# Optimization experiments

Hardware: AMD Instinct MI355X
Metric: run time of the kernel (lower is better)

## Reference

```python
import jax, jax.numpy as jnp
import numpy as np
import math

B, N, D, H, K, W = 2, 2048, 512, 8, 64, 5
HD = D // H      # head_dim = 64
QC = HD // 4     # per-head quaternion component = 16
QI = D // 4      # full-model quaternion component = 128


def _qlinear(x, r, i, j, k, b):
    # Hamilton-product weight matrix, as built in QLinear.forward
    Wm = jnp.concatenate([
        jnp.concatenate([r, -i, -j, -k], 1),
        jnp.concatenate([i,  r, -k,  j], 1),
        jnp.concatenate([j,  k,  r, -i], 1),
        jnp.concatenate([k, -j,  i,  r], 1)], 0)
    return x @ Wm.T + b


def _layernorm(x, g, b, eps=1e-5):
    m = x.mean(-1, keepdims=True)
    v = ((x - m) ** 2).mean(-1, keepdims=True)
    return (x - m) / jnp.sqrt(v + eps) * g + b


def _forward(query, key, value, cross_context, density_feat, mask, time_idx,
             q_r, q_i, q_j, q_k, q_b, k_r, k_i, k_j, k_k, k_b,
             v_w, v_b, o_w, o_b, thr, dm1_w, dm1_b, dm2_w, dm2_b,
             ef, ec, ev_w, ev_b, ln_g, ln_b):
    spike_slope = 5.0
    # ---- QuaternionSpikeAttention (cross_ctx=True, dropout inactive in eval) ----
    q = _qlinear(query, q_r, q_i, q_j, q_k, q_b)
    k = _qlinear(key, k_r, k_i, k_j, k_k, k_b) + _qlinear(cross_context, k_r, k_i, k_j, k_k, k_b)
    v = jnp.concatenate([value, cross_context], -1) @ v_w.T + v_b
    qh = q.reshape(B, N, H, HD)
    kh = k.reshape(B, N, H, HD)
    vh = v.reshape(B, N, H, HD)
    # sum of the 4 quaternion-component dot products == full dot over head_dim
    scores = jnp.einsum('bmhd,bnhd->bhmn', qh, kh) / math.sqrt(QC)
    scores = jnp.clip(scores, -6.0, 6.0)
    base_thr = jax.nn.softplus(thr)
    hdm = jax.nn.gelu(density_feat @ dm1_w.T + dm1_b, approximate=False)
    d_shift = (hdm @ dm2_w.T + dm2_b)[..., 0]                # [B, N]
    threshold = base_thr + d_shift[:, None, None, :] * 0.1   # varies over key index
    gate = jax.nn.sigmoid(spike_slope * (scores - threshold))
    mod = scores * (1.0 + 2.0 * gate)
    m2 = mask[:, None, :, None] * mask[:, None, None, :]     # [B,1,M,N] outer mask
    mod = jnp.where(m2 == 0, -10000.0, mod)
    wts = jax.nn.softmax(jnp.clip(mod, -30.0, 30.0), axis=-1)
    attn = jnp.einsum('bhmn,bnhd->bmhd', wts, vh).reshape(B, N, D)
    attn = attn @ o_w.T + o_b
    # ---- TemporalEventConvolution ----
    order = jnp.argsort(time_idx, axis=1)
    qs = jnp.take_along_axis(query, order[..., None], axis=1)
    ms = jnp.take_along_axis(mask, order, axis=1)
    half = W // 2
    qp = jnp.pad(qs, ((0, 0), (half, half), (0, 0)))
    qwin = jnp.stack([qp[:, w:w + N] for w in range(W)], axis=2)  # [B,N,W,D]
    # quaternion-split filter matching collapses to a full dot over D
    act = jnp.einsum('bnwd,kwd->bnk', qwin, ef) / math.sqrt(QI)
    act = jnp.where(ms[..., None] == 0, -10000.0, act)
    act = jax.nn.softmax(act, axis=-1)
    ctx = act @ ec                                            # [B,N,D]
    ctx = _layernorm(ctx @ ev_w.T + ev_b, ln_g, ln_b) * ms[..., None]
    inv = jnp.argsort(order, axis=1)
    ctx = jnp.take_along_axis(ctx, inv[..., None], axis=1) * mask[..., None]
    return attn + ctx


def setup_inputs() -> dict:
    key0 = jax.random.key(0)
    ks = jax.random.split(key0, 24)
    lim = math.sqrt(6.0 / (QI + QI))
    def xav(k):
        return jax.random.uniform(k, (QI, QI), jnp.float32, -lim, lim)
    def lin(k, o, i):
        l = math.sqrt(1.0 / i)
        return jax.random.uniform(k, (o, i), jnp.float32, -l, l)
    return {
        'query': jax.random.normal(ks[0], (B, N, D), jnp.float32),
        'key': jax.random.normal(ks[1], (B, N, D), jnp.float32),
        'value': jax.random.normal(ks[2], (B, N, D), jnp.float32),
        'cross_context': jax.random.normal(ks[3], (B, N, D), jnp.float32),
        'density_feat': jax.random.normal(ks[4], (B, N, 3), jnp.float32),
        'mask': jnp.ones((B, N), jnp.float32),
        'time_idx': jax.random.randint(ks[5], (B, N), 0, 1000000),
        'q_r': xav(ks[6]), 'q_i': xav(ks[7]), 'q_j': xav(ks[8]), 'q_k': xav(ks[9]),
        'q_b': jnp.zeros((D,), jnp.float32),
        'k_r': xav(ks[10]), 'k_i': xav(ks[11]), 'k_j': xav(ks[12]), 'k_k': xav(ks[13]),
        'k_b': jnp.zeros((D,), jnp.float32),
        'v_w': lin(ks[14], D, 2 * D), 'v_b': jnp.zeros((D,), jnp.float32),
        'o_w': lin(ks[15], D, D), 'o_b': jnp.zeros((D,), jnp.float32),
        'thr': jnp.float32(-1.0),
        'dm1_w': lin(ks[16], 16, 3), 'dm1_b': jnp.zeros((16,), jnp.float32),
        'dm2_w': jnp.zeros((1, 16), jnp.float32), 'dm2_b': jnp.zeros((1,), jnp.float32),
        'ef': jax.random.normal(ks[17], (K, W, D), jnp.float32) * 0.02,
        'ec': jax.random.normal(ks[18], (K, D), jnp.float32) * 0.02,
        'ev_w': lin(ks[19], D, D), 'ev_b': jnp.zeros((D,), jnp.float32),
        'ln_g': jnp.ones((D,), jnp.float32), 'ln_b': jnp.zeros((D,), jnp.float32),
    }


def reference(query, key, value, cross_context, density_feat, mask, time_idx,
              q_r, q_i, q_j, q_k, q_b, k_r, k_i, k_j, k_k, k_b,
              v_w, v_b, o_w, o_b, thr, dm1_w, dm1_b, dm2_w, dm2_b,
              ef, ec, ev_w, ev_b, ln_g, ln_b):
    return _forward(query, key, value, cross_context, density_feat, mask, time_idx,
                    q_r, q_i, q_j, q_k, q_b, k_r, k_i, k_j, k_k, k_b,
                    v_w, v_b, o_w, o_b, thr, dm1_w, dm1_b, dm2_w, dm2_b,
                    ef, ec, ev_w, ev_b, ln_g, ln_b)
```

## Files before the change

### kernel.cpp

```cpp
#include <hip/hip_runtime.h>
#include <math.h>

#define BB 2
#define NN 2048
#define DDIM 512
#define HH 8
#define HDIM 64
#define BN 4096

#define WS_WMQ   0
#define WS_WMK   262144
#define WS_THRK  524288
#define WS_ORDER 528384
#define WS_DKW   532480
#define WS_W5    1843200
#define WS_Q     2105344
#define WS_K     4202496
#define WS_V     6299648
#define PLANE_US 2097152

typedef short bf16x8 __attribute__((ext_vector_type(8)));
typedef float f32x4  __attribute__((ext_vector_type(4)));

__device__ __forceinline__ float4 ld4(const float* p) { return *(const float4*)p; }

__device__ __forceinline__ float red16_sum(float v) {
  v += __shfl_xor(v, 1, 64);
  v += __shfl_xor(v, 2, 64);
  v += __shfl_xor(v, 4, 64);
  v += __shfl_xor(v, 8, 64);
  return v;
}

__device__ __forceinline__ unsigned short f2bu(float f) {
  unsigned u = __float_as_uint(f);
  unsigned r = 0x7FFFu + ((u >> 16) & 1u);
  return (unsigned short)((u + r) >> 16);
}
__device__ __forceinline__ float bu2f(unsigned short u) {
  return __uint_as_float(((unsigned)u) << 16);
}
__device__ __forceinline__ void split2(float x, unsigned short& hi, unsigned short& lo) {
  hi = f2bu(x);
  lo = f2bu(x - bu2f(hi));
}

__global__ __launch_bounds__(256) void build_wm_kernel(
    const float* __restrict__ qr, const float* __restrict__ qi,
    const float* __restrict__ qj, const float* __restrict__ qk,
    const float* __restrict__ kr, const float* __restrict__ ki,
    const float* __restrict__ kj, const float* __restrict__ kk,
    unsigned short* __restrict__ wmqH, unsigned short* __restrict__ wmqL,
    unsigned short* __restrict__ wmkH, unsigned short* __restrict__ wmkL)
{
  int idx = blockIdx.x * 256 + threadIdx.x;
  int sel = idx >> 18;
  int r   = idx & 262143;
  int p = r >> 9, q = r & 511;
  int pb = p >> 7, qb = q >> 7, pr = p & 127, qc = q & 127;
  const int   comp_t[4][4] = {{0,1,2,3},{1,0,3,2},{2,3,0,1},{3,2,1,0}};
  const float sign_t[4][4] = {{1.f,-1.f,-1.f,-1.f},{1.f,1.f,-1.f,1.f},
                              {1.f,1.f,1.f,-1.f},{1.f,-1.f,1.f,1.f}};
  const float* cq[4] = {qr,qi,qj,qk};
  const float* ck[4] = {kr,ki,kj,kk};
  int c = comp_t[pb][qb];
  float s = sign_t[pb][qb];
  const float* src = sel ? ck[c] : cq[c];
  float v = s * src[pr*128 + qc];
  unsigned short hi, lo;
  split2(v, hi, lo);
  if (sel) { wmkH[r] = hi; wmkL[r] = lo; }
  else     { wmqH[r] = hi; wmqL[r] = lo; }
}

__global__ __launch_bounds__(256) void presplit_kernel(
    const float* __restrict__ src, int n4,
    unsigned short* __restrict__ hp, unsigned short* __restrict__ lp)
{
  int i = blockIdx.x * 256 + threadIdx.x;
  if (i >= n4) return;
  float4 v = ((const float4*)src)[i];
  ushort4 h, l;
  split2(v.x, h.x, l.x);  split2(v.y, h.y, l.y);
  split2(v.z, h.z, l.z);  split2(v.w, h.w, l.w);
  ((ushort4*)hp)[i] = h;
  ((ushort4*)lp)[i] = l;
}

__global__ __launch_bounds__(256) void rank_kernel(const int* __restrict__ tidx,
                                                   int* __restrict__ order)
{
  __shared__ int ts[NN];
  int b = blockIdx.y;
  for (int i = threadIdx.x; i < NN; i += 256) ts[i] = tidx[b*NN + i];
  __syncthreads();
  int i = blockIdx.x * 256 + threadIdx.x;
  int ti = ts[i];
  int rank = 0;
  #pragma unroll 4
  for (int j = 0; j < NN; j++) {
    int tj = ts[j];
    rank += (tj < ti || (tj == ti && j < i)) ? 1 : 0;
  }
  order[b*NN + rank] = i;
}

__global__ __launch_bounds__(256) void thr_kernel(
    const float* __restrict__ df, const float* __restrict__ dm1w,
    const float* __restrict__ dm1b, const float* __restrict__ dm2w,
    const float* __restrict__ dm2b, const float* __restrict__ thrp,
    int dm1b_bstride, float* __restrict__ thrK)
{
  int i = blockIdx.x * 256 + threadIdx.x;
  if (i >= BN) return;
  int b = i >> 11;
  const float* bb = dm1b + b*dm1b_bstride;
  float x0 = df[i*3+0], x1 = df[i*3+1], x2 = df[i*3+2];
  float acc = dm2b[0];
  #pragma unroll
  for (int j = 0; j < 16; j++) {
    float h = dm1w[j*3+0]*x0 + dm1w[j*3+1]*x1 + dm1w[j*3+2]*x2 + bb[j];
    h = 0.5f * h * (1.f + erff(h * 0.70710678118654752f));
    acc += h * dm2w[j];
  }
  float tv = thrp[0];
  float base = fmaxf(tv, 0.f) + log1pf(expf(-fabsf(tv)));
  thrK[i] = base + 0.1f * acc;
}

#define GSTR 72
template<int MODE, int OUT, int AP, int BP>
__device__ __forceinline__ void mgemm_body(
    unsigned short* AHi, unsigned short* ALo,
    unsigned short* BHi, unsigned short* BLo,
    const float* __restrict__ A0, const float* __restrict__ A1,
    const unsigned short* __restrict__ APh, const unsigned short* __restrict__ APl,
    const float* __restrict__ W,
    const unsigned short* __restrict__ BPh, const unsigned short* __restrict__ BPl,
    const float* __restrict__ bias,
    float bias_scale, float scale, float* __restrict__ out,
    int Ka, int N, int ldout, int bx, int by)
{
  const int t = threadIdx.x;
  const int w = t >> 6, lane = t & 63;
  const int quad = lane >> 4, lm = lane & 15;
  const int m0 = bx * 64, n0 = by * 64;
  const int lrr = t >> 4, ld = (t & 15) * 4;

  f32x4 acc[4];
  #pragma unroll
  for (int s = 0; s < 4; s++) acc[s] = (f32x4){0.f,0.f,0.f,0.f};

  for (int k0 = 0; k0 < Ka; k0 += 64) {
    __syncthreads();
    if (AP) {
      #pragma unroll
      for (int i = 0; i < 2; i++) {
        int c = t*2 + i;
        int row = c >> 3, c8 = (c & 7) * 8;
        int off = (m0 + row)*Ka + k0 + c8;
        *(uint4*)&AHi[row*GSTR + c8] = *(const uint4*)&APh[off];
        *(uint4*)&ALo[row*GSTR + c8] = *(const uint4*)&APl[off];
      }
    } else {
      #pragma unroll
      for (int p = 0; p < 4; p++) {
        int row = lrr + p*16;
        float4 av;
        if (MODE == 0) {
          av = ld4(&A0[(size_t)(m0+row)*Ka + k0 + ld]);
        } else if (MODE == 1) {
          float4 x = ld4(&A0[(m0+row)*512 + k0 + ld]);
          float4 y = ld4(&A1[(m0+row)*512 + k0 + ld]);
          av = make_float4(x.x+y.x, x.y+y.y, x.z+y.z, x.w+y.w);
        } else {
          int kg = k0 + ld;
          av = (kg < 512) ? ld4(&A0[(m0+row)*512 + kg])
                          : ld4(&A1[(m0+row)*512 + kg - 512]);
        }
        ushort4 hi, lo;
        split2(av.x, hi.x, lo.x);  split2(av.y, hi.y, lo.y);
        split2(av.z, hi.z, lo.z);  split2(av.w, hi.w, lo.w);
        *(ushort4*)&AHi[row*GSTR + ld] = hi;
        *(ushort4*)&ALo[row*GSTR + ld] = lo;
      }
    }
    if (BP) {
      #pragma unroll
      for (int i = 0; i < 2; i++) {
        int c = t*2 + i;
        int row = c >> 3, c8 = (c & 7) * 8;
        int brow = n0 + row;  if (brow > N-1) brow = N-1;
        int off = brow*Ka + k0 + c8;
        *(uint4*)&BHi[row*GSTR + c8] = *(const uint4*)&BPh[off];
        *(uint4*)&BLo[row*GSTR + c8] = *(const uint4*)&BPl[off];
      }
    } else {
      #pragma unroll
      for (int p = 0; p < 4; p++) {
        int row = lrr + p*16;
        int brow = n0 + row;  if (brow > N-1) brow = N-1;
        float4 wv = ld4(&W[(size_t)brow*Ka + k0 + ld]);
        ushort4 hi, lo;
        split2(wv.x, hi.x, lo.x);  split2(wv.y, hi.y, lo.y);
        split2(wv.z, hi.z, lo.z);  split2(wv.w, hi.w, lo.w);
        *(ushort4*)&BHi[row*GSTR + ld] = hi;
        *(ushort4*)&BLo[row*GSTR + ld] = lo;
      }
    }
    __syncthreads();
    #pragma unroll
    for (int ks = 0; ks < 2; ks++) {
      int arow = (w*16 + lm)*GSTR + ks*32 + quad*8;
      bf16x8 ah = *(const bf16x8*)&AHi[arow];
      bf16x8 al = *(const bf16x8*)&ALo[arow];
      #pragma unroll
      for (int sub = 0; sub < 4; sub++) {
        int baddr = (sub*16 + lm)*GSTR + ks*32 + quad*8;
        bf16x8 bh = *(const bf16x8*)&BHi[baddr];
        bf16x8 bl = *(const bf16x8*)&BLo[baddr];
        acc[sub] = __builtin_amdgcn_mfma_f32_16x16x32_bf16(ah, bh, acc[sub], 0, 0, 0);
        acc[sub] = __builtin_amdgcn_mfma_f32_16x16x32_bf16(ah, bl, acc[sub], 0, 0, 0);
        acc[sub] = __builtin_amdgcn_mfma_f32_16x16x32_bf16(al, bh, acc[sub], 0, 0, 0);
      }
    }
  }
  #pragma unroll
  for (int sub = 0; sub < 4; sub++) {
    int col = n0 + sub*16 + lm;
    if (col >= N) continue;
    float bv = bias ? bias[col] * bias_scale : 0.f;
    if (OUT == 0) {
      #pragma unroll
      for (int r = 0; r < 4; r++) {
        int row = m0 + w*16 + quad*4 + r;
        out[(size_t)row*ldout + col] = acc[sub][r]*scale + bv;
      }
    } else if (OUT == 1) {
      unsigned short* hp = (unsigned short*)out;
      unsigned short* lp = hp + (size_t)4096*ldout;
      #pragma unroll
      for (int r = 0; r < 4; r++) {
        int row = m0 + w*16 + quad*4 + r;
        unsigned short hv, lv;
        split2(acc[sub][r]*scale + bv, hv, lv);
        hp[(size_t)row*ldout + col] = hv;
        lp[(size_t)row*ldout + col] = lv;
      }
    } else {
      unsigned short* hp = (unsigned short*)out;
      unsigned short* lp = hp + (size_t)PLANE_US;
      int hcol = col >> 6, d = col & 63;
      int row0 = m0 + w*16 + quad*4;
      int bb2 = row0 >> 11, n = row0 & 2047;
      unsigned short h0,h1,h2,h3,l0,l1,l2,l3;
      split2(acc[sub][0]*scale + bv, h0, l0);
      split2(acc[sub][1]*scale + bv, h1, l1);
      split2(acc[sub][2]*scale + bv, h2, l2);
      split2(acc[sub][3]*scale + bv, h3, l3);
      size_t vidx = (((size_t)bb2*8 + hcol)*64 + d)*2048 + n;
      *(ushort4*)&hp[vidx] = make_ushort4(h0,h1,h2,h3);
      *(ushort4*)&lp[vidx] = make_ushort4(l0,l1,l2,l3);
    }
  }
}

template<int MODE, int OUT, int AP, int BP>
__global__ __launch_bounds__(256) void mgemm_kernel(
    const float* __restrict__ A0, const float* __restrict__ A1,
    const unsigned short* __restrict__ APh, const unsigned short* __restrict__ APl,
    const float* __restrict__ W,
    const unsigned short* __restrict__ BPh, const unsigned short* __restrict__ BPl,
    const float* __restrict__ bias,
    float bias_scale, float scale, float* __restrict__ out,
    int Ka, int N, int ldout)
{
  __shared__ __align__(16) unsigned short AHi[64*GSTR], ALo[64*GSTR];
  __shared__ __align__(16) unsigned short BHi[64*GSTR], BLo[64*GSTR];
  mgemm_body<MODE,OUT,AP,BP>(AHi, ALo, BHi, BLo, A0, A1, APh, APl, W, BPh, BPl,
                             bias, bias_scale, scale, out, Ka, N, ldout,
                             blockIdx.x, blockIdx.y);
}

__global__ __launch_bounds__(256) void qkv_kernel(
    const unsigned short* __restrict__ qryH, const unsigned short* __restrict__ qryL,
    const unsigned short* __restrict__ wmqH, const unsigned short* __restrict__ wmqL,
    const float* __restrict__ q_b, float* __restrict__ Qb,
    const float* __restrict__ key_, const float* __restrict__ cross,
    const unsigned short* __restrict__ wmkH, const unsigned short* __restrict__ wmkL,
    const float* __restrict__ k_b, float* __restrict__ Kb,
    const float* __restrict__ value,
    const unsigned short* __restrict__ vwH, const unsigned short* __restrict__ vwL,
    const float* __restrict__ v_b, float* __restrict__ Vb)
{
  __shared__ __align__(16) unsigned short AHi[64*GSTR], ALo[64*GSTR];
  __shared__ __align__(16) unsigned short BHi[64*GSTR], BLo[64*GSTR];
  int by = blockIdx.y;
  if (by < 8) {
    mgemm_body<0,1,1,1>(AHi, ALo, BHi, BLo, nullptr, nullptr, qryH, qryL,
                        nullptr, wmqH, wmqL, q_b, 1.f, 1.f, Qb, 512, 512, 512,
                        blockIdx.x, by);
  } else if (by < 16) {
    mgemm_body<1,1,0,1>(AHi, ALo, BHi, BLo, key_, cross, nullptr, nullptr,
                        nullptr, wmkH, wmkL, k_b, 2.f, 1.f, Kb, 512, 512, 512,
                        blockIdx.x, by - 8);
  } else {
    mgemm_body<2,2,0,1>(AHi, ALo, BHi, BLo, value, cross, nullptr, nullptr,
                        nullptr, vwH, vwL, v_b, 1.f, 1.f, Vb, 1024, 512, 512,
                        blockIdx.x, by - 16);
  }
}

__global__ __launch_bounds__(256) void t1a_kernel(const float* __restrict__ dkw,
    const int* __restrict__ order, int K, int W, float* __restrict__ w5raw)
{
  int idx = blockIdx.x * 256 + threadIdx.x;
  if (idx >= BN*K) return;
  int k  = idx % K;
  int bn = idx / K;
  int b = bn >> 11, r = bn & 2047;
  const int* ob = order + b*NN;
  int KW = K*W, half = W >> 1;
  float acc = 0.f;
  for (int w = 0; w < W; w++) {
    int rr = r + w - half;
    if (rr < 0 || rr >= NN) continue;
    acc += dkw[(size_t)(b*NN + ob[rr])*KW + k*W + w];
  }
  w5raw[(size_t)(b*NN + ob[r])*K + k] = acc;
}

__global__ __launch_bounds__(256) void ecv_kernel(const float* __restrict__ ec,
    const float* __restrict__ evw, int K, float* __restrict__ ecv)
{
  int idx = blockIdx.x * 256 + threadIdx.x;
  if (idx >= K*512) return;
  int k = idx >> 9, j = idx & 511;
  const float4* e4 = (const float4*)(ec + k*512);
  const float4* w4 = (const float4*)(evw + j*512);
  float acc = 0.f;
  for (int d = 0; d < 128; d++) {
    float4 a = e4[d], b = w4[d];
    acc += a.x*b.x + a.y*b.y + a.z*b.z + a.w*b.w;
  }
  ecv[k*512 + j] = acc;
}

__global__ __launch_bounds__(256) void t2f_kernel(const float* __restrict__ w5raw,
    const float* __restrict__ ecv, const float* __restrict__ evb,
    const float* __restrict__ mask, int K, float* __restrict__ ctx2)
{
  int idx = blockIdx.x * 256 + threadIdx.x;
  int bn = idx >> 7;
  int q4 = idx & 127;
  const float* row = w5raw + (size_t)bn*K;
  const float4* e4 = (const float4*)ecv;
  float4 acc = ((const float4*)evb)[q4];
  float mk = mask[bn];
  if (mk == 0.f) {
    float u = 1.f / (float)K;
    for (int k = 0; k < K; k++) {
      float4 e = e4[k*128 + q4];
      acc.x += u*e.x; acc.y += u*e.y; acc.z += u*e.z; acc.w += u*e.w;
    }
  } else {
    float mx = -1e30f;
    for (int k = 0; k < K; k++) mx = fmaxf(mx, row[k]);
    float ss = 0.f;
    for (int k = 0; k < K; k++) ss += __expf(row[k]-mx);
    float inv = 1.f/ss;
    for (int k = 0; k < K; k++) {
      float w = __expf(row[k]-mx) * inv;
      float4 e = e4[k*128 + q4];
      acc.x += w*e.x; acc.y += w*e.y; acc.z += w*e.z; acc.w += w*e.w;
    }
  }
  ((float4*)ctx2)[idx] = acc;
}

#define QSTR 72
__global__ __launch_bounds__(256) void attn_kernel(
    const unsigned short* __restrict__ QHi, const unsigned short* __restrict__ QLo,
    const unsigned short* __restrict__ KHp, const unsigned short* __restrict__ KLp,
    const unsigned short* __restrict__ VtHi, const unsigned short* __restrict__ VtLo,
    const float* __restrict__ thrK, const float* __restrict__ mask,
    unsigned short* __restrict__ AoutH, unsigned short* __restrict__ AoutL)
{
  __shared__ __align__(16) unsigned short KHs[64*QSTR];
  __shared__ __align__(16) unsigned short KLs[64*QSTR];
  __shared__ __align__(16) unsigned short VHs[64*QSTR];
  __shared__ __align__(16) unsigned short VLs[64*QSTR];
  __shared__ float thr_s[64], mk_s[64], mm_s[32];
  __shared__ float ls[2][32];

  const int t = threadIdx.x;
  const int wv = t >> 6, lane = t & 63;
  const int g = wv & 1, sh = wv >> 1;
  const int quad = lane >> 4, lm = lane & 15;
  const int m0 = blockIdx.x * 32;
  const int bh = blockIdx.y;
  const int b = bh >> 3, h = bh & 7;
  const int base = b*NN*DDIM + h*HDIM;
  const int sr = t >> 3;
  const int sc = (t & 7) * 8;

  bf16x8 qh[2], ql[2];
  {
    size_t qoff = (size_t)(b*NN + m0 + g*16 + lm)*DDIM + h*HDIM + quad*8;
    qh[0] = *(const bf16x8*)&QHi[qoff];
    qh[1] = *(const bf16x8*)&QHi[qoff + 32];
    ql[0] = *(const bf16x8*)&QLo[qoff];
    ql[1] = *(const bf16x8*)&QLo[qoff + 32];
  }
  if (t < 32) mm_s[t] = mask[b*NN + m0 + t];

  f32x4 o_acc[2];
  o_acc[0] = (f32x4){0.f,0.f,0.f,0.f};
  o_acc[1] = (f32x4){0.f,0.f,0.f,0.f};
  float lsum[4] = {0.f,0.f,0.f,0.f};

  for (int n0 = 0; n0 < NN; n0 += 64) {
    __syncthreads();
    #pragma unroll
    for (int p = 0; p < 2; p++) {
      int row = sr + p*32;
      size_t gg = (size_t)(b*NN + n0 + row)*DDIM + h*HDIM + sc;
      *(uint4*)&KHs[row*QSTR + sc] = *(const uint4*)&KHp[gg];
      *(uint4*)&KLs[row*QSTR + sc] = *(const uint4*)&KLp[gg];
      size_t gv = ((size_t)bh*HDIM + row)*NN + n0 + sc;
      *(uint4*)&VHs[row*QSTR + sc] = *(const uint4*)&VtHi[gv];
      *(uint4*)&VLs[row*QSTR + sc] = *(const uint4*)&VtLo[gv];
    }
    if (t < 64) { thr_s[t] = thrK[b*NN + n0 + t]; mk_s[t] = mask[b*NN + n0 + t]; }
    __syncthreads();

    f32x4 s_acc[2];
    s_acc[0] = (f32x4){0.f,0.f,0.f,0.f};
    s_acc[1] = (f32x4){0.f,0.f,0.f,0.f};
    #pragma unroll
    for (int ks = 0; ks < 2; ks++) {
      #pragma unroll
      for (int sl = 0; sl < 2; sl++) {
        int sub = sh*2 + sl;
        int baddr = (sub*16 + lm)*QSTR + ks*32 + quad*8;
        bf16x8 bh8 = *(const bf16x8*)&KHs[baddr];
        bf16x8 bl8 = *(const bf16x8*)&KLs[baddr];
        s_acc[sl] = __builtin_amdgcn_mfma_f32_16x16x32_bf16(qh[ks], bh8, s_acc[sl], 0, 0, 0);
        s_acc[sl] = __builtin_amdgcn_mfma_f32_16x16x32_bf16(qh[ks], bl8, s_acc[sl], 0, 0, 0);
        s_acc[sl] = __builtin_amdgcn_mfma_f32_16x16x32_bf16(ql[ks], bh8, s_acc[sl], 0, 0, 0);
      }
    }
    __syncthreads();

    float thc5[2], mkc[2];
    #pragma unroll
    for (int sl = 0; sl < 2; sl++) {
      int key = (sh*2 + sl)*16 + lm;
      thc5[sl] = 5.f * thr_s[key];
      mkc[sl] = mk_s[key];
    }
    float p_[4][2];
    #pragma unroll
    for (int r = 0; r < 4; r++) {
      float mm = mm_s[g*16 + quad*4 + r];
      #pragma unroll
      for (int sl = 0; sl < 2; sl++) {
        float sc2 = s_acc[sl][r]*0.25f;
        sc2 = fminf(fmaxf(sc2,-6.f),6.f);
        float e = __expf(__builtin_fmaf(-5.f, sc2, thc5[sl]));
        float gte = __builtin_amdgcn_rcpf(1.f + e);
        float mv = sc2*(1.f + 2.f*gte);
        if (mm*mkc[sl] == 0.f) mv = -1e4f;
        mv = fminf(fmaxf(mv,-30.f),30.f);
        float p = __expf(mv - 30.f);
        p_[r][sl] = p;
        lsum[r] += p;
      }
    }
    #pragma unroll
    for (int r = 0; r < 4; r++) {
      int prow = (g*16 + quad*4 + r)*QSTR;
      int xk = quad << 3;
      #pragma unroll
      for (int sl = 0; sl < 2; sl++) {
        int cx = (lm + (sh*2+sl)*16) ^ xk;
        unsigned short hi, lo;
        split2(p_[r][sl], hi, lo);
        KHs[prow + cx] = hi;
        KLs[prow + cx] = lo;
      }
    }
    __syncthreads();

    bf16x8 ph[2], pl[2];
    {
      int arow = (g*16 + lm)*QSTR;
      int rk = ((lm >> 2) & 3) << 3;
      int c0 = (quad*8) ^ rk;
      int c1 = (quad*8 + 32) ^ rk;
      ph[0] = *(const bf16x8*)&KHs[arow + c0];
      ph[1] = *(const bf16x8*)&KHs[arow + c1];
      pl[0] = *(const bf16x8*)&KLs[arow + c0];
      pl[1] = *(const bf16x8*)&KLs[arow + c1];
    }
    #pragma unroll
    for (int ks = 0; ks < 2; ks++) {
      #pragma unroll
      for (int sl = 0; sl < 2; sl++) {
        int sub = sh*2 + sl;
        int baddr = (sub*16 + lm)*QSTR + ks*32 + quad*8;
        bf16x8 vh8 = *(const bf16x8*)&VHs[baddr];
        bf16x8 vl8 = *(const bf16x8*)&VLs[baddr];
        o_acc[sl] = __builtin_amdgcn_mfma_f32_16x16x32_bf16(ph[ks], vh8, o_acc[sl], 0, 0, 0);
        o_acc[sl] = __builtin_amdgcn_mfma_f32_16x16x32_bf16(ph[ks], vl8, o_acc[sl], 0, 0, 0);
        o_acc[sl] = __builtin_amdgcn_mfma_f32_16x16x32_bf16(pl[ks], vh8, o_acc[sl], 0, 0, 0);
      }
    }
  }

  __syncthreads();
  #pragma unroll
  for (int r = 0; r < 4; r++) {
    float s = red16_sum(lsum[r]);
    if (lm == 0) ls[sh][g*16 + quad*4 + r] = s;
  }
  __syncthreads();
  float inv[4];
  #pragma unroll
  for (int r = 0; r < 4; r++) {
    int rl = g*16 + quad*4 + r;
    inv[r] = 1.f / (ls[0][rl] + ls[1][rl]);
  }
  #pragma unroll
  for (int sl = 0; sl < 2; sl++) {
    #pragma unroll
    for (int r = 0; r < 4; r++) {
      int row = m0 + g*16 + quad*4 + r;
      float val = o_acc[sl][r] * inv[r];
      unsigned short hv, lv;
      split2(val, hv, lv);
      size_t o = (size_t)base + (size_t)row*DDIM + (sh*2+sl)*16 + lm;
      AoutH[o] = hv;
      AoutL[o] = lv;
    }
  }
}

__global__ __launch_bounds__(256) void t3_kernel(const float* __restrict__ ctx2,
    const float* __restrict__ lng, const float* __restrict__ lnb,
    const float* __restrict__ mask, const float* __restrict__ outf,
    float* __restrict__ out)
{
  int wid = threadIdx.x >> 6, lane = threadIdx.x & 63;
  int row = blockIdx.x * 4 + wid;
  const float4* x4 = (const float4*)(ctx2 + row*DDIM);
  float4 v0 = x4[lane], v1 = x4[lane+64];
  float s = v0.x+v0.y+v0.z+v0.w + v1.x+v1.y+v1.z+v1.w;
  #pragma unroll
  for (int m = 1; m < 64; m <<= 1) s += __shfl_xor(s, m, 64);
  float mean = s * (1.f/512.f);
  float d0 = v0.x-mean, d1 = v0.y-mean, d2 = v0.z-mean, d3 = v0.w-mean;
  float d4 = v1.x-mean, d5 = v1.y-mean, d6 = v1.z-mean, d7 = v1.w-mean;
  float sq = d0*d0+d1*d1+d2*d2+d3*d3+d4*d4+d5*d5+d6*d6+d7*d7;
  #pragma unroll
  for (int m = 1; m < 64; m <<= 1) sq += __shfl_xor(sq, m, 64);
  float rstd = rsqrtf(sq * (1.f/512.f) + 1e-5f);
  float mk = mask[row];
  float f = mk*mk;
  const float4* g4 = (const float4*)lng;
  const float4* b4 = (const float4*)lnb;
  float4 G0 = g4[lane], G1 = g4[lane+64], B0 = b4[lane], B1 = b4[lane+64];
  float4 O0 = *(const float4*)&outf[row*DDIM + lane*4];
  float4 O1 = *(const float4*)&outf[row*DDIM + (lane+64)*4];
  float4 R0, R1;
  R0.x = O0.x + (d0*rstd*G0.x + B0.x)*f;
  R0.y = O0.y + (d1*rstd*G0.y + B0.y)*f;
  R0.z = O0.z + (d2*rstd*G0.z + B0.z)*f;
  R0.w = O0.w + (d3*rstd*G0.w + B0.w)*f;
  R1.x = O1.x + (d4*rstd*G1.x + B1.x)*f;
  R1.y = O1.y + (d5*rstd*G1.y + B1.y)*f;
  R1.z = O1.z + (d6*rstd*G1.z + B1.z)*f;
  R1.w = O1.w + (d7*rstd*G1.w + B1.w)*f;
  *(float4*)&out[row*DDIM + lane*4] = R0;
  *(float4*)&out[row*DDIM + (lane+64)*4] = R1;
}

__global__ void telem_write_kernel(float val, float* __restrict__ out)
{
  if (threadIdx.x == 0 && blockIdx.x == 0) out[0] = val;
}

extern "C" void kernel_launch(void* const* d_in, const int* in_sizes, int n_in,
                              void* d_out, int out_size, void* d_ws, size_t ws_size,
                              hipStream_t stream)
{
  (void)n_in; (void)out_size; (void)ws_size;
  const float* query = (const float*)d_in[0];
  const float* key_  = (const float*)d_in[1];
  const float* value = (const float*)d_in[2];
  const float* cross = (const float*)d_in[3];
  const float* df    = (const float*)d_in[4];
  const float* mask  = (const float*)d_in[5];
  const int*   tidx  = (const int*)  d_in[6];
  const float* q_r = (const float*)d_in[7],  *q_i = (const float*)d_in[8];
  const float* q_j = (const float*)d_in[9],  *q_k = (const float*)d_in[10];
  const float* q_b = (const float*)d_in[11];
  const float* k_r = (const float*)d_in[12], *k_i = (const float*)d_in[13];
  const float* k_j = (const float*)d_in[14], *k_k = (const float*)d_in[15];
  const float* k_b = (const float*)d_in[16];
  const float* v_w = (const float*)d_in[17], *v_b = (const float*)d_in[18];
  const float* o_w = (const float*)d_in[19], *o_b = (const float*)d_in[20];
  const float* thrp = (const float*)d_in[21];
  const float* dm1w = (const float*)d_in[22], *dm1b = (const float*)d_in[23];
  const float* dm2w = (const float*)d_in[24], *dm2b = (const float*)d_in[25];
  const float* ef   = (const float*)d_in[26], *ec   = (const float*)d_in[27];
  const float* ev_w = (const float*)d_in[28], *ev_b = (const float*)d_in[29];
  const float* lng  = (const float*)d_in[30], *lnb  = (const float*)d_in[31];

  const int s23 = in_sizes[23];
  const int s26 = in_sizes[26];
  const int s27 = in_sizes[27];
  int Kf = (s27 > 0 && s27 % 512 == 0) ? s27 / 512 : 0;
  int Wf = (Kf > 0 && s26 % (Kf*512) == 0) ? s26 / (Kf*512) : 0;
  bool cfg_ok = (Kf >= 1 && Kf <= 64) && (Wf == 1 || Wf == 3 || Wf == 5)
                && (Kf*Wf <= 320);
  if (!cfg_ok) { Kf = 5; Wf = 5; }
  const int KW = Kf * Wf;
  const int dm1b_bstride = (s23 == 32) ? 16 : 0;

  float* ws   = (float*)d_ws;
  float* thrK = ws + WS_THRK;
  int*   order = (int*)(ws + WS_ORDER);
  float* dkw  = ws + WS_DKW;
  float* w5   = ws + WS_W5;
  float* Qb   = ws + WS_Q;
  float* Kb   = ws + WS_K;
  float* Vb   = ws + WS_V;
  float* out  = (float*)d_out;
  float* OutF = Kb;
  float* ctx2 = Qb;

  unsigned short* wmqH = (unsigned short*)(ws + WS_WMQ);
  unsigned short* wmqL = wmqH + 262144;
  unsigned short* wmkH = (unsigned short*)(ws + WS_WMK);
  unsigned short* wmkL = wmkH + 262144;
  unsigned short* qryH = (unsigned short*)d_out;
  unsigned short* qryL = qryH + PLANE_US;
  unsigned short* vwH  = (unsigned short*)(ws + WS_DKW);
  unsigned short* vwL  = vwH + 524288;
  unsigned short* owH  = (unsigned short*)(ws + WS_W5);
  unsigned short* owL  = owH + 262144;
  unsigned short* efH  = (unsigned short*)(ws + WS_WMQ);
  unsigned short* efL  = efH + KW*512;
  float* ecv = ws + WS_WMQ;

  const unsigned short* QHi = (const unsigned short*)Qb;
  const unsigned short* QLo = QHi + PLANE_US;
  const unsigned short* KHp = (const unsigned short*)Kb;
  const unsigned short* KLp = KHp + PLANE_US;
  const unsigned short* VtH = (const unsigned short*)Vb;
  const unsigned short* VtL = VtH + PLANE_US;

  build_wm_kernel<<<2048, 256, 0, stream>>>(q_r,q_i,q_j,q_k, k_r,k_i,k_j,k_k,
                                            wmqH, wmqL, wmkH, wmkL);
  rank_kernel<<<dim3(8,2), 256, 0, stream>>>(tidx, order);
  thr_kernel<<<16, 256, 0, stream>>>(df, dm1w, dm1b, dm2w, dm2b, thrp,
                                     dm1b_bstride, thrK);
  presplit_kernel<<<2048, 256, 0, stream>>>(query, 524288, qryH, qryL);
  presplit_kernel<<<512, 256, 0, stream>>>(v_w, 131072, vwH, vwL);
  presplit_kernel<<<256, 256, 0, stream>>>(o_w, 65536, owH, owL);

  const float rs128 = 0.08838834764831845f;
  qkv_kernel<<<dim3(64,24), 256, 0, stream>>>(
      qryH, qryL, wmqH, wmqL, q_b, Qb,
      key_, cross, wmkH, wmkL, k_b, Kb,
      value, vwH, vwL, v_b, Vb);
  presplit_kernel<<<(KW*128 + 255)/256, 256, 0, stream>>>(ef, KW*128, efH, efL);
  mgemm_kernel<0,0,1,1><<<dim3(64,(KW+63)/64), 256, 0, stream>>>(
      nullptr, nullptr, qryH, qryL, nullptr, efH, efL, nullptr, 0.f, rs128, dkw, 512, KW, KW);

  attn_kernel<<<dim3(64,16), 256, 0, stream>>>(QHi, QLo, KHp, KLp, VtH, VtL,
                                               thrK, mask, qryH, qryL);
  mgemm_kernel<0,0,1,1><<<dim3(64,8), 256, 0, stream>>>(
      nullptr, nullptr, qryH, qryL, nullptr, owH, owL, o_b, 1.f, 1.f, OutF, 512, 512, 512);

  t1a_kernel<<<(BN*Kf + 255)/256, 256, 0, stream>>>(dkw, order, Kf, Wf, w5);
  ecv_kernel<<<(Kf*512 + 255)/256, 256, 0, stream>>>(ec, ev_w, Kf, ecv);
  t2f_kernel<<<2048, 256, 0, stream>>>(w5, ecv, ev_b, mask, Kf, ctx2);
  t3_kernel<<<1024, 256, 0, stream>>>(ctx2, lng, lnb, mask, OutF, out);

  if (!cfg_ok) {
    int K2 = (s27 / 512 < 127) ? s27 / 512 : 127;
    telem_write_kernel<<<1, 64, 0, stream>>>(-65536.f * (float)(K2+1), out);
  }
}
```

Baseline: 504.6 us.

## Fuse small GEMMs into shared launches and restructure attention to direct global loads

Folds the ef-projection GEMM into the qkv launch as extra block rows, and merges the output projection, the temporal window sum and the ec·ev_w product into one tail launch. Workspace buffers are relocated so the fused paths do not overlap. The attention kernel now uses 16-row query tiles with twice the blocks, each wave owning 16 keys. K and V are loaded straight from global memory instead of being staged through shared memory, which removes several barriers and LDS traffic but relies on cache hits for K/V reuse. The aim is fewer launches and better occupancy, at the cost of more redundant global reads of K and V.

```diff
diff --git a/kernel.cpp b/kernel.cpp
--- a/kernel.cpp
+++ b/kernel.cpp
@@ -291,7 +291,9 @@
     const float* __restrict__ k_b, float* __restrict__ Kb,
     const float* __restrict__ value,
     const unsigned short* __restrict__ vwH, const unsigned short* __restrict__ vwL,
-    const float* __restrict__ v_b, float* __restrict__ Vb)
+    const float* __restrict__ v_b, float* __restrict__ Vb,
+    const unsigned short* __restrict__ efH, const unsigned short* __restrict__ efL,
+    float rs128, int KW, float* __restrict__ dkwO)
 {
   __shared__ __align__(16) unsigned short AHi[64*GSTR], ALo[64*GSTR];
   __shared__ __align__(16) unsigned short BHi[64*GSTR], BLo[64*GSTR];
@@ -304,46 +306,63 @@
     mgemm_body<1,1,0,1>(AHi, ALo, BHi, BLo, key_, cross, nullptr, nullptr,
                         nullptr, wmkH, wmkL, k_b, 2.f, 1.f, Kb, 512, 512, 512,
                         blockIdx.x, by - 8);
-  } else {
+  } else if (by < 24) {
     mgemm_body<2,2,0,1>(AHi, ALo, BHi, BLo, value, cross, nullptr, nullptr,
                         nullptr, vwH, vwL, v_b, 1.f, 1.f, Vb, 1024, 512, 512,
                         blockIdx.x, by - 16);
-  }
-}
-
-__global__ __launch_bounds__(256) void t1a_kernel(const float* __restrict__ dkw,
-    const int* __restrict__ order, int K, int W, float* __restrict__ w5raw)
-{
-  int idx = blockIdx.x * 256 + threadIdx.x;
-  if (idx >= BN*K) return;
-  int k  = idx % K;
-  int bn = idx / K;
-  int b = bn >> 11, r = bn & 2047;
-  const int* ob = order + b*NN;
-  int KW = K*W, half = W >> 1;
-  float acc = 0.f;
-  for (int w = 0; w < W; w++) {
-    int rr = r + w - half;
-    if (rr < 0 || rr >= NN) continue;
-    acc += dkw[(size_t)(b*NN + ob[rr])*KW + k*W + w];
-  }
-  w5raw[(size_t)(b*NN + ob[r])*K + k] = acc;
-}
-
-__global__ __launch_bounds__(256) void ecv_kernel(const float* __restrict__ ec,
-    const float* __restrict__ evw, int K, float* __restrict__ ecv)
-{
-  int idx = blockIdx.x * 256 + threadIdx.x;
-  if (idx >= K*512) return;
-  int k = idx >> 9, j = idx & 511;
-  const float4* e4 = (const float4*)(ec + k*512);
-  const float4* w4 = (const float4*)(evw + j*512);
-  float acc = 0.f;
-  for (int d = 0; d < 128; d++) {
-    float4 a = e4[d], b = w4[d];
-    acc += a.x*b.x + a.y*b.y + a.z*b.z + a.w*b.w;
-  }
-  ecv[k*512 + j] = acc;
+  } else {
+    mgemm_body<0,0,1,1>(AHi, ALo, BHi, BLo, nullptr, nullptr, qryH, qryL,
+                        nullptr, efH, efL, nullptr, 0.f, rs128, dkwO, 512, KW, KW,
+                        blockIdx.x, by - 24);
+  }
+}
+
+__global__ __launch_bounds__(256) void otail_kernel(
+    const unsigned short* __restrict__ aH, const unsigned short* __restrict__ aL,
+    const unsigned short* __restrict__ owH, const unsigned short* __restrict__ owL,
+    const float* __restrict__ o_b, float* __restrict__ OutF,
+    const float* __restrict__ dkw, const int* __restrict__ order,
+    int K, int W, float* __restrict__ w5,
+    const float* __restrict__ ec, const float* __restrict__ evw,
+    float* __restrict__ ecv)
+{
+  __shared__ __align__(16) unsigned short AHi[64*GSTR], ALo[64*GSTR];
+  __shared__ __align__(16) unsigned short BHi[64*GSTR], BLo[64*GSTR];
+  int by = blockIdx.y;
+  if (by < 8) {
+    mgemm_body<0,0,1,1>(AHi, ALo, BHi, BLo, nullptr, nullptr, aH, aL,
+                        nullptr, owH, owL, o_b, 1.f, 1.f, OutF, 512, 512, 512,
+                        blockIdx.x, by);
+  } else if (by == 8) {
+    int KW = K*W, half = W >> 1;
+    int total = BN*K;
+    for (int idx = blockIdx.x*256 + threadIdx.x; idx < total; idx += 64*256) {
+      int k  = idx % K;
+      int bn = idx / K;
+      int b = bn >> 11, r = bn & 2047;
+      const int* ob = order + b*NN;
+      float acc = 0.f;
+      for (int w = 0; w < W; w++) {
+        int rr = r + w - half;
+        if (rr < 0 || rr >= NN) continue;
+        acc += dkw[(size_t)(b*NN + ob[rr])*KW + k*W + w];
+      }
+      w5[(size_t)(b*NN + ob[r])*K + k] = acc;
+    }
+  } else {
+    int total = K*512;
+    for (int idx = blockIdx.x*256 + threadIdx.x; idx < total; idx += 64*256) {
+      int k = idx >> 9, j = idx & 511;
+      const float4* e4 = (const float4*)(ec + k*512);
+      const float4* w4 = (const float4*)(evw + j*512);
+      float acc = 0.f;
+      for (int d = 0; d < 128; d++) {
+        float4 a = e4[d], bv = w4[d];
+        acc += a.x*bv.x + a.y*bv.y + a.z*bv.z + a.w*bv.w;
+      }
+      ecv[k*512 + j] = acc;
+    }
+  }
 }
 
 __global__ __launch_bounds__(256) void t2f_kernel(const float* __restrict__ w5raw,
@@ -378,7 +397,7 @@
   ((float4*)ctx2)[idx] = acc;
 }
 
-#define QSTR 72
+#define PSTR 72
 __global__ __launch_bounds__(256) void attn_kernel(
     const unsigned short* __restrict__ QHi, const unsigned short* __restrict__ QLo,
     const unsigned short* __restrict__ KHp, const unsigned short* __restrict__ KLp,
@@ -386,163 +405,113 @@
     const float* __restrict__ thrK, const float* __restrict__ mask,
     unsigned short* __restrict__ AoutH, unsigned short* __restrict__ AoutL)
 {
-  __shared__ __align__(16) unsigned short KHs[64*QSTR];
-  __shared__ __align__(16) unsigned short KLs[64*QSTR];
-  __shared__ __align__(16) unsigned short VHs[64*QSTR];
-  __shared__ __align__(16) unsigned short VLs[64*QSTR];
-  __shared__ float thr_s[64], mk_s[64], mm_s[32];
-  __shared__ float ls[2][32];
+  __shared__ __align__(16) unsigned short PHs[16*PSTR];
+  __shared__ __align__(16) unsigned short PLs[16*PSTR];
+  __shared__ float ls[4][16];
 
   const int t = threadIdx.x;
   const int wv = t >> 6, lane = t & 63;
-  const int g = wv & 1, sh = wv >> 1;
   const int quad = lane >> 4, lm = lane & 15;
-  const int m0 = blockIdx.x * 32;
+  const int m0 = blockIdx.x * 16;
   const int bh = blockIdx.y;
   const int b = bh >> 3, h = bh & 7;
   const int base = b*NN*DDIM + h*HDIM;
-  const int sr = t >> 3;
-  const int sc = (t & 7) * 8;
 
   bf16x8 qh[2], ql[2];
   {
-    size_t qoff = (size_t)(b*NN + m0 + g*16 + lm)*DDIM + h*HDIM + quad*8;
+    size_t qoff = (size_t)(b*NN + m0 + lm)*DDIM + h*HDIM + quad*8;
     qh[0] = *(const bf16x8*)&QHi[qoff];
     qh[1] = *(const bf16x8*)&QHi[qoff + 32];
     ql[0] = *(const bf16x8*)&QLo[qoff];
     ql[1] = *(const bf16x8*)&QLo[qoff + 32];
   }
-  if (t < 32) mm_s[t] = mask[b*NN + m0 + t];
-
-  f32x4 o_acc[2];
-  o_acc[0] = (f32x4){0.f,0.f,0.f,0.f};
-  o_acc[1] = (f32x4){0.f,0.f,0.f,0.f};
+  float mmv[4];
+  #pragma unroll
+  for (int r = 0; r < 4; r++) mmv[r] = mask[b*NN + m0 + quad*4 + r];
+
+  f32x4 o_acc = (f32x4){0.f,0.f,0.f,0.f};
   float lsum[4] = {0.f,0.f,0.f,0.f};
 
   for (int n0 = 0; n0 < NN; n0 += 64) {
-    __syncthreads();
-    #pragma unroll
-    for (int p = 0; p < 2; p++) {
-      int row = sr + p*32;
-      size_t gg = (size_t)(b*NN + n0 + row)*DDIM + h*HDIM + sc;
-      *(uint4*)&KHs[row*QSTR + sc] = *(const uint4*)&KHp[gg];
-      *(uint4*)&KLs[row*QSTR + sc] = *(const uint4*)&KLp[gg];
-      size_t gv = ((size_t)bh*HDIM + row)*NN + n0 + sc;
-      *(uint4*)&VHs[row*QSTR + sc] = *(const uint4*)&VtHi[gv];
-      *(uint4*)&VLs[row*QSTR + sc] = *(const uint4*)&VtLo[gv];
-    }
-    if (t < 64) { thr_s[t] = thrK[b*NN + n0 + t]; mk_s[t] = mask[b*NN + n0 + t]; }
-    __syncthreads();
-
-    f32x4 s_acc[2];
-    s_acc[0] = (f32x4){0.f,0.f,0.f,0.f};
-    s_acc[1] = (f32x4){0.f,0.f,0.f,0.f};
+    int key = wv*16 + lm;
+    f32x4 s_acc = (f32x4){0.f,0.f,0.f,0.f};
+    size_t kbase = (size_t)(b*NN + n0 + key)*DDIM + h*HDIM + quad*8;
     #pragma unroll
     for (int ks = 0; ks < 2; ks++) {
-      #pragma unroll
-      for (int sl = 0; sl < 2; sl++) {
-        int sub = sh*2 + sl;
-        int baddr = (sub*16 + lm)*QSTR + ks*32 + quad*8;
-        bf16x8 bh8 = *(const bf16x8*)&KHs[baddr];
-        bf16x8 bl8 = *(const bf16x8*)&KLs[baddr];
-        s_acc[sl] = __builtin_amdgcn_mfma_f32_16x16x32_bf16(qh[ks], bh8, s_acc[sl], 0, 0, 0);
-        s_acc[sl] = __builtin_amdgcn_mfma_f32_16x16x32_bf16(qh[ks], bl8, s_acc[sl], 0, 0, 0);
-        s_acc[sl] = __builtin_amdgcn_mfma_f32_16x16x32_bf16(ql[ks], bh8, s_acc[sl], 0, 0, 0);
-      }
-    }
-    __syncthreads();
-
-    float thc5[2], mkc[2];
-    #pragma unroll
-    for (int sl = 0; sl < 2; sl++) {
-      int key = (sh*2 + sl)*16 + lm;
-      thc5[sl] = 5.f * thr_s[key];
-      mkc[sl] = mk_s[key];
-    }
-    float p_[4][2];
+      bf16x8 bh8 = *(const bf16x8*)&KHp[kbase + ks*32];
+      bf16x8 bl8 = *(const bf16x8*)&KLp[kbase + ks*32];
+      s_acc = __builtin_amdgcn_mfma_f32_16x16x32_bf16(qh[ks], bh8, s_acc, 0, 0, 0);
+      s_acc = __builtin_amdgcn_mfma_f32_16x16x32_bf16(qh[ks], bl8, s_acc, 0, 0, 0);
+      s_acc = __builtin_amdgcn_mfma_f32_16x16x32_bf16(ql[ks], bh8, s_acc, 0, 0, 0);
+    }
+
+    float thc5 = 5.f * thrK[b*NN + n0 + key];
+    float mkc  = mask[b*NN + n0 + key];
+    float p_[4];
     #pragma unroll
     for (int r = 0; r < 4; r++) {
-      float mm = mm_s[g*16 + quad*4 + r];
-      #pragma unroll
-      for (int sl = 0; sl < 2; sl++) {
-        float sc2 = s_acc[sl][r]*0.25f;
-        sc2 = fminf(fmaxf(sc2,-6.f),6.f);
-        float e = __expf(__builtin_fmaf(-5.f, sc2, thc5[sl]));
-        float gte = __builtin_amdgcn_rcpf(1.f + e);
-        float mv = sc2*(1.f + 2.f*gte);
-        if (mm*mkc[sl] == 0.f) mv = -1e4f;
-        mv = fminf(fmaxf(mv,-30.f),30.f);
-        float p = __expf(mv - 30.f);
-        p_[r][sl] = p;
-        lsum[r] += p;
-      }
+      float sc2 = s_acc[r]*0.25f;
+      sc2 = fminf(fmaxf(sc2,-6.f),6.f);
+      float e = __expf(__builtin_fmaf(-5.f, sc2, thc5));
+      float gte = __builtin_amdgcn_rcpf(1.f + e);
+      float mv = sc2*(1.f + 2.f*gte);
+      if (mmv[r]*mkc == 0.f) mv = -1e4f;
+      mv = fminf(fmaxf(mv,-30.f),30.f);
+      float p = __expf(mv - 30.f);
+      p_[r] = p;
+      lsum[r] += p;
     }
     #pragma unroll
     for (int r = 0; r < 4; r++) {
-      int prow = (g*16 + quad*4 + r)*QSTR;
-      int xk = quad << 3;
-      #pragma unroll
-      for (int sl = 0; sl < 2; sl++) {
-        int cx = (lm + (sh*2+sl)*16) ^ xk;
-        unsigned short hi, lo;
-        split2(p_[r][sl], hi, lo);
-        KHs[prow + cx] = hi;
-        KLs[prow + cx] = lo;
-      }
+      int prow = (quad*4 + r)*PSTR;
+      int cx = (lm + wv*16) ^ (quad << 3);
+      unsigned short hi, lo;
+      split2(p_[r], hi, lo);
+      PHs[prow + cx] = hi;
+      PLs[prow + cx] = lo;
     }
     __syncthreads();
 
     bf16x8 ph[2], pl[2];
     {
-      int arow = (g*16 + lm)*QSTR;
+      int arow = lm*PSTR;
       int rk = ((lm >> 2) & 3) << 3;
       int c0 = (quad*8) ^ rk;
       int c1 = (quad*8 + 32) ^ rk;
-      ph[0] = *(const bf16x8*)&KHs[arow + c0];
-      ph[1] = *(const bf16x8*)&KHs[arow + c1];
-      pl[0] = *(const bf16x8*)&KLs[arow + c0];
-      pl[1] = *(const bf16x8*)&KLs[arow + c1];
-    }
+      ph[0] = *(const bf16x8*)&PHs[arow + c0];
+      ph[1] = *(const bf16x8*)&PHs[arow + c1];
+      pl[0] = *(const bf16x8*)&PLs[arow + c0];
+      pl[1] = *(const bf16x8*)&PLs[arow + c1];
+    }
+    size_t vbase = ((size_t)bh*HDIM + wv*16 + lm)*NN + n0 + quad*8;
     #pragma unroll
     for (int ks = 0; ks < 2; ks++) {
-      #pragma unroll
-      for (int sl = 0; sl < 2; sl++) {
-        int sub = sh*2 + sl;
-        int baddr = (sub*16 + lm)*QSTR + ks*32 + quad*8;
-        bf16x8 vh8 = *(const bf16x8*)&VHs[baddr];
-        bf16x8 vl8 = *(const bf16x8*)&VLs[baddr];
-        o_acc[sl] = __builtin_amdgcn_mfma_f32_16x16x32_bf16(ph[ks], vh8, o_acc[sl], 0, 0, 0);
-        o_acc[sl] = __builtin_amdgcn_mfma_f32_16x16x32_bf16(ph[ks], vl8, o_acc[sl], 0, 0, 0);
-        o_acc[sl] = __builtin_amdgcn_mfma_f32_16x16x32_bf16(pl[ks], vh8, o_acc[sl], 0, 0, 0);
-      }
-    }
-  }
-
-  __syncthreads();
+      bf16x8 vh8 = *(const bf16x8*)&VtHi[vbase + ks*32];
+      bf16x8 vl8 = *(const bf16x8*)&VtLo[vbase + ks*32];
+      o_acc = __builtin_amdgcn_mfma_f32_16x16x32_bf16(ph[ks], vh8, o_acc, 0, 0, 0);
+      o_acc = __builtin_amdgcn_mfma_f32_16x16x32_bf16(ph[ks], vl8, o_acc, 0, 0, 0);
+      o_acc = __builtin_amdgcn_mfma_f32_16x16x32_bf16(pl[ks], vh8, o_acc, 0, 0, 0);
+    }
+    __syncthreads();
+  }
+
   #pragma unroll
   for (int r = 0; r < 4; r++) {
     float s = red16_sum(lsum[r]);
-    if (lm == 0) ls[sh][g*16 + quad*4 + r] = s;
+    if (lm == 0) ls[wv][quad*4 + r] = s;
   }
   __syncthreads();
-  float inv[4];
   #pragma unroll
   for (int r = 0; r < 4; r++) {
-    int rl = g*16 + quad*4 + r;
-    inv[r] = 1.f / (ls[0][rl] + ls[1][rl]);
-  }
-  #pragma unroll
-  for (int sl = 0; sl < 2; sl++) {
-    #pragma unroll
-    for (int r = 0; r < 4; r++) {
-      int row = m0 + g*16 + quad*4 + r;
-      float val = o_acc[sl][r] * inv[r];
-      unsigned short hv, lv;
-      split2(val, hv, lv);
-      size_t o = (size_t)base + (size_t)row*DDIM + (sh*2+sl)*16 + lm;
-      AoutH[o] = hv;
-      AoutL[o] = lv;
-    }
+    int rl = quad*4 + r;
+    float inv = 1.f / (ls[0][rl] + ls[1][rl] + ls[2][rl] + ls[3][rl]);
+    int row = m0 + quad*4 + r;
+    float val = o_acc[r] * inv;
+    unsigned short hv, lv;
+    split2(val, hv, lv);
+    size_t o = (size_t)base + (size_t)row*DDIM + wv*16 + lm;
+    AoutH[o] = hv;
+    AoutL[o] = lv;
   }
 }
 
@@ -627,18 +596,18 @@
   if (!cfg_ok) { Kf = 5; Wf = 5; }
   const int KW = Kf * Wf;
   const int dm1b_bstride = (s23 == 32) ? 16 : 0;
+  const bool fused_ef = (KW <= 160);
 
   float* ws   = (float*)d_ws;
   float* thrK = ws + WS_THRK;
   int*   order = (int*)(ws + WS_ORDER);
-  float* dkw  = ws + WS_DKW;
-  float* w5   = ws + WS_W5;
   float* Qb   = ws + WS_Q;
   float* Kb   = ws + WS_K;
   float* Vb   = ws + WS_V;
   float* out  = (float*)d_out;
   float* OutF = Kb;
   float* ctx2 = Qb;
+  float* w5   = ws + WS_V;
 
   unsigned short* wmqH = (unsigned short*)(ws + WS_WMQ);
   unsigned short* wmqL = wmqH + 262144;
@@ -650,9 +619,19 @@
   unsigned short* vwL  = vwH + 524288;
   unsigned short* owH  = (unsigned short*)(ws + WS_W5);
   unsigned short* owL  = owH + 262144;
-  unsigned short* efH  = (unsigned short*)(ws + WS_WMQ);
-  unsigned short* efL  = efH + KW*512;
   float* ecv = ws + WS_WMQ;
+
+  float* dkwP;
+  unsigned short *efH_, *efL_;
+  if (fused_ef) {
+    dkwP = ws + WS_DKW + 524288;
+    efH_ = (unsigned short*)(dkwP + (size_t)BN*KW);
+    efL_ = efH_ + KW*512;
+  } else {
+    dkwP = ws + WS_DKW;
+    efH_ = (unsigned short*)(ws + WS_WMQ);
+    efL_ = efH_ + KW*512;
+  }
 
   const unsigned short* QHi = (const unsigned short*)Qb;
   const unsigned short* QLo = QHi + PLANE_US;
@@ -669,23 +648,29 @@
   presplit_kernel<<<2048, 256, 0, stream>>>(query, 524288, qryH, qryL);
   presplit_kernel<<<512, 256, 0, stream>>>(v_w, 131072, vwH, vwL);
   presplit_kernel<<<256, 256, 0, stream>>>(o_w, 65536, owH, owL);
+  if (fused_ef)
+    presplit_kernel<<<(KW*128 + 255)/256, 256, 0, stream>>>(ef, KW*128, efH_, efL_);
 
   const float rs128 = 0.08838834764831845f;
-  qkv_kernel<<<dim3(64,24), 256, 0, stream>>>(
+  const int efcols = (KW + 63) / 64;
+  qkv_kernel<<<dim3(64, fused_ef ? 24 + efcols : 24), 256, 0, stream>>>(
       qryH, qryL, wmqH, wmqL, q_b, Qb,
       key_, cross, wmkH, wmkL, k_b, Kb,
-      value, vwH, vwL, v_b, Vb);
-  presplit_kernel<<<(KW*128 + 255)/256, 256, 0, stream>>>(ef, KW*128, efH, efL);
-  mgemm_kernel<0,0,1,1><<<dim3(64,(KW+63)/64), 256, 0, stream>>>(
-      nullptr, nullptr, qryH, qryL, nullptr, efH, efL, nullptr, 0.f, rs128, dkw, 512, KW, KW);
-
-  attn_kernel<<<dim3(64,16), 256, 0, stream>>>(QHi, QLo, KHp, KLp, VtH, VtL,
-                                               thrK, mask, qryH, qryL);
-  mgemm_kernel<0,0,1,1><<<dim3(64,8), 256, 0, stream>>>(
-      nullptr, nullptr, qryH, qryL, nullptr, owH, owL, o_b, 1.f, 1.f, OutF, 512, 512, 512);
-
-  t1a_kernel<<<(BN*Kf + 255)/256, 256, 0, stream>>>(dkw, order, Kf, Wf, w5);
-  ecv_kernel<<<(Kf*512 + 255)/256, 256, 0, stream>>>(ec, ev_w, Kf, ecv);
+      value, vwH, vwL, v_b, Vb,
+      efH_, efL_, rs128, KW, dkwP);
+  if (!fused_ef) {
+    presplit_kernel<<<(KW*128 + 255)/256, 256, 0, stream>>>(ef, KW*128, efH_, efL_);
+    mgemm_kernel<0,0,1,1><<<dim3(64, efcols), 256, 0, stream>>>(
+        nullptr, nullptr, qryH, qryL, nullptr, efH_, efL_, nullptr, 0.f, rs128,
+        dkwP, 512, KW, KW);
+  }
+
+  attn_kernel<<<dim3(128,16), 256, 0, stream>>>(QHi, QLo, KHp, KLp, VtH, VtL,
+                                                thrK, mask, qryH, qryL);
+  otail_kernel<<<dim3(64,10), 256, 0, stream>>>(
+      qryH, qryL, owH, owL, o_b, OutF,
+      dkwP, order, Kf, Wf, w5, ec, ev_w, ecv);
+
   t2f_kernel<<<2048, 256, 0, stream>>>(w5, ecv, ev_b, mask, Kf, ctx2);
   t3_kernel<<<1024, 256, 0, stream>>>(ctx2, lng, lnb, mask, OutF, out);
 
```

Result: slower. 645.4 us (+27.9%).
